# Kernel optimization log

Measured on AMD Instinct MI355X. Metric: run time of the kernel, lower is better.

Reference implementation:

```python
import jax, jax.numpy as jnp
import numpy as np

# AdEx constants (match init_kwargs)
THR = -50.4
EL = -70.6
GL = 30.0
C = 281.0
DELTAT = 2.0
V_RESET = -70.6
TAUW = 144.0
A = 4.0
B = 0.0805
DT = 1.0
N_REFRAC = 5
DAMP = 0.3
DT_GL__C = DT * GL / C
DT_A__TAUW = DT * A / TAUW

BATCH, N_IN, UNITS = 8192, 256, 1024


@jax.custom_vjp
def spike_function(v_scaled):
    return (v_scaled > 0.0).astype(jnp.float32)

def _spike_fwd(v_scaled):
    return spike_function(v_scaled), v_scaled

def _spike_bwd(v_scaled, dy):
    # pseudo-derivative: dampening * max(1 - |v_scaled|, 0)
    return (dy * DAMP * jnp.maximum(1.0 - jnp.abs(v_scaled), 0.0),)

spike_function.defvjp(_spike_fwd, _spike_bwd)


def setup_inputs() -> dict:
    key = jax.random.key(0)
    ks = jax.random.split(key, 7)
    inputs = jax.random.normal(ks[0], (BATCH, N_IN), dtype=jnp.float32)
    old_v = EL + 5.0 * jax.random.normal(ks[1], (BATCH, UNITS), dtype=jnp.float32)
    old_r = jax.random.randint(ks[2], (BATCH, UNITS), 0, N_REFRAC, dtype=jnp.int32)
    old_w = jax.random.normal(ks[3], (BATCH, UNITS), dtype=jnp.float32)
    old_z = (jax.random.uniform(ks[4], (BATCH, UNITS)) < 0.1).astype(jnp.float32)
    input_weights = jax.random.uniform(ks[5], (N_IN, UNITS), dtype=jnp.float32, minval=0.0, maxval=1.2)
    recurrent_weights = 0.7 * jax.random.normal(ks[6], (UNITS, UNITS), dtype=jnp.float32) / np.sqrt(UNITS)
    return {"inputs": inputs, "old_v": old_v, "old_r": old_r, "old_w": old_w,
            "old_z": old_z, "input_weights": input_weights,
            "recurrent_weights": recurrent_weights}


def reference(inputs, old_v, old_r, old_w, old_z, input_weights, recurrent_weights):
    units = recurrent_weights.shape[0]
    disconnect = jnp.eye(units, dtype=bool)  # no autapses on diagonal
    no_autapse_w_rec = jnp.where(disconnect, 0.0, recurrent_weights)

    i_t = inputs @ input_weights + old_z @ no_autapse_w_rec  # (B, U)

    exp_terms = jnp.clip(jnp.exp((old_v - THR) / DELTAT), -1e6, 30.0 / DT_GL__C)
    exp_terms = jax.lax.stop_gradient(exp_terms)

    new_v = (old_v - DT_GL__C * (old_v - EL)
             + DT_GL__C * DELTAT * exp_terms
             + (i_t - old_w) * DT / C)
    new_v = jnp.where(old_z > 0.5, V_RESET, new_v)

    new_w = old_w - DT / TAUW * old_w + DT_A__TAUW * (old_v - EL) + B * old_z

    is_refractory = old_r > 0
    v_scaled = -(THR - new_v) / (THR - EL)
    new_z = spike_function(v_scaled)
    new_z = jnp.where(is_refractory, 0.0, new_z)

    new_r = jnp.clip(old_r - 1 + (new_z * N_REFRAC).astype(jnp.int32), 0, N_REFRAC)

    return new_v, new_z, new_r, new_w
```

## Files before the change

kernel.cpp:

```cpp
#include <hip/hip_runtime.h>
#include <stdint.h>

#define THRC      (-50.4f)
#define ELC       (-70.6f)
#define V_RESETC  (-70.6f)
#define DT_GL_C   (0.10676156583629893f)
#define DELTATC   (2.0f)
#define DT_C      (0.0035587188612099642f)
#define DT_TAUW   (0.006944444444444444f)
#define DTA_TAUW  (0.027777777777777776f)
#define BCONST    (0.0805f)
#define EXPCLIP   (281.0f)

#define M_TOT 8192
#define UNITS 1024
#define KX    768
#define KBT   1792
#define CH    (8192*1024)
#define BM 256
#define BN 128
#define ZSLAB (M_TOT*16)

typedef __attribute__((ext_vector_type(8))) short s16x8;
typedef __attribute__((ext_vector_type(4))) float f32x4;

__device__ __forceinline__ unsigned short f2bf(float f) {
  union { float f; unsigned int u; } v; v.f = f;
  unsigned int r = v.u + 0x7fffu + ((v.u >> 16) & 1u);
  return (unsigned short)(r >> 16);
}
__device__ __forceinline__ float bf2f(unsigned short h) {
  union { unsigned int u; float f; } v; v.u = ((unsigned int)h) << 16; return v.f;
}
__device__ __forceinline__ void gload_lds16(const void* g, void* l) {
  __builtin_amdgcn_global_load_lds(
      (const __attribute__((address_space(1))) void*)g,
      (__attribute__((address_space(3))) void*)l, 16, 0, 0);
}
__device__ __forceinline__ int swz_col(int row, int k) {
  return (k & ~31) | (((((k >> 3) & 3) ^ ((row >> 1) & 3)) << 3)) | (k & 7);
}

__global__ __launch_bounds__(256) void build_ax(const float* __restrict__ X,
                                                unsigned short* __restrict__ AX) {
  int o = blockIdx.x * 256 + threadIdx.x;
  int row = o / 96;
  int c8 = (o - row * 96) * 8;
  const float* src; bool lo = false;
  if (c8 < 256)        { src = X + (size_t)row * 256 + c8; }
  else if (c8 < 512)   { src = X + (size_t)row * 256 + (c8 - 256); lo = true; }
  else                 { src = X + (size_t)row * 256 + (c8 - 512); }
  float4 f0 = *(const float4*)(src);
  float4 f1 = *(const float4*)(src + 4);
  float fv[8] = {f0.x, f0.y, f0.z, f0.w, f1.x, f1.y, f1.z, f1.w};
  unsigned short h[8];
#pragma unroll
  for (int i = 0; i < 8; ++i) {
    unsigned short hi = f2bf(fv[i]);
    h[i] = lo ? f2bf(fv[i] - bf2f(hi)) : hi;
  }
  uint4 pk;
  pk.x = (unsigned)h[0] | ((unsigned)h[1] << 16);
  pk.y = (unsigned)h[2] | ((unsigned)h[3] << 16);
  pk.z = (unsigned)h[4] | ((unsigned)h[5] << 16);
  pk.w = (unsigned)h[6] | ((unsigned)h[7] << 16);
  *(uint4*)(AX + (size_t)row * KX + swz_col(row, c8)) = pk;
}

__global__ __launch_bounds__(256) void build_b(const float* __restrict__ Wi,
                                               const float* __restrict__ Wr,
                                               unsigned short* __restrict__ BT) {
  __shared__ unsigned short tile[32][33];
  int tx = threadIdx.x & 31, ty = threadIdx.x >> 5;
  int k0 = blockIdx.x * 32, n0 = blockIdx.y * 32;
#pragma unroll
  for (int j = 0; j < 4; ++j) {
    int kk = k0 + ty + j * 8;
    int n  = n0 + tx;
    float f; bool lo = false;
    if (kk < 256)       f = Wi[(size_t)kk * 1024 + n];
    else if (kk < 512)  f = Wi[(size_t)(kk - 256) * 1024 + n];
    else if (kk < 768) { f = Wi[(size_t)(kk - 512) * 1024 + n]; lo = true; }
    else { int kr = kk - 768; f = (kr == n) ? 0.0f : Wr[(size_t)kr * 1024 + n]; }
    unsigned short h = f2bf(f);
    if (lo) h = f2bf(f - bf2f(h));
    tile[ty + j * 8][tx] = h;
  }
  __syncthreads();
#pragma unroll
  for (int j = 0; j < 4; ++j) {
    int n  = n0 + ty + j * 8;
    int kk = k0 + tx;
    BT[(size_t)n * KBT + swz_col(n, kk)] = tile[tx][ty + j * 8];
  }
}

__global__ __launch_bounds__(256) void build_zb(const float* __restrict__ Z,
                                                char* __restrict__ Zb) {
  int ge = blockIdx.x * 256 + threadIdx.x;
  float val = Z[ge];
  unsigned long long mask = __ballot(val > 0.5f);
  if ((threadIdx.x & 63) == 0) {
    int row = ge >> 10;
    int k0  = ge & 1023;
    *(unsigned long long*)(Zb + (size_t)(k0 >> 7) * ZSLAB + row * 16 + ((k0 >> 3) & 15)) = mask;
  }
}

__device__ __forceinline__ s16x8 expand_bits(unsigned zw, int l4) {
  unsigned b = zw >> (l4 * 8);
  s16x8 a;
#pragma unroll
  for (int e = 0; e < 8; ++e)
    a[e] = (short)(((b >> e) & 1u) ? 0x3F80 : 0);
  return a;
}

__global__ __launch_bounds__(512, 2) void adex_gemm(
    const unsigned short* __restrict__ AX, const unsigned short* __restrict__ BT,
    const char* __restrict__ Zb,
    const float* __restrict__ oV, const int* __restrict__ oR,
    const float* __restrict__ oW, float* __restrict__ out)
{
  __shared__ unsigned short S[2][12288];
  const int tid  = threadIdx.x;
  const int w    = tid >> 6;
  const int lane = tid & 63;
  const int l15  = lane & 15, l4 = lane >> 4;
  const int wm   = w >> 1, wn = w & 1;

  const int bid = blockIdx.x;
  const int mt = bid >> 3, nt = bid & 7;
  const int rowA0 = mt * BM;
  const int colB0 = nt * BN;

  const int srow = tid >> 2, sslot = tid & 3;
  const unsigned short* aS0 = AX + (size_t)(rowA0 + srow)       * KX  + sslot * 8;
  const unsigned short* aS1 = AX + (size_t)(rowA0 + 128 + srow) * KX  + sslot * 8;
  const unsigned short* bS  = BT + (size_t)(colB0 + srow)       * KBT + sslot * 8;

#define STAGE_A(buf)                                          \
  do { gload_lds16(aS0, &S[buf][0] + tid * 8);                \
       gload_lds16(aS1, &S[buf][0] + 4096 + tid * 8); } while (0)
#define STAGE_B(buf) gload_lds16(bS, &S[buf][0] + 8192 + tid * 8)

  const int slot = l4 ^ ((l15 >> 1) & 3);
  int offA[4], offB[4];
#pragma unroll
  for (int f = 0; f < 4; ++f) offA[f] = (wm * 64 + f * 16 + l15) * 32 + slot * 8;
#pragma unroll
  for (int f = 0; f < 4; ++f) offB[f] = 8192 + (wn * 64 + f * 16 + l15) * 32 + slot * 8;

  const char* zp0 = Zb + (size_t)(rowA0 + wm * 64 +  0 + l15) * 16;
  const char* zp1 = Zb + (size_t)(rowA0 + wm * 64 + 16 + l15) * 16;
  const char* zp2 = Zb + (size_t)(rowA0 + wm * 64 + 32 + l15) * 16;
  const char* zp3 = Zb + (size_t)(rowA0 + wm * 64 + 48 + l15) * 16;

  f32x4 acc[4][4];
#pragma unroll
  for (int i = 0; i < 4; ++i)
#pragma unroll
    for (int j = 0; j < 4; ++j) acc[i][j] = (f32x4){0.f, 0.f, 0.f, 0.f};

  STAGE_A(0); STAGE_B(0);
  uint4 zbE0 = *(const uint4*)zp0, zbE1 = *(const uint4*)zp1;
  uint4 zbE2 = *(const uint4*)zp2, zbE3 = *(const uint4*)zp3;
  asm volatile("s_waitcnt vmcnt(0)" ::: "memory");
  __syncthreads();

  int cur = 0;
#pragma unroll 2
  for (int ks = 0; ks < 24; ++ks) {
    if (ks < 23) { aS0 += 32; aS1 += 32; bS += 32; STAGE_A(cur ^ 1); STAGE_B(cur ^ 1); }
    else         { bS += 32; STAGE_B(cur ^ 1); }
    const unsigned short* base = &S[cur][0];
    s16x8 af[4], bf[4];
#pragma unroll
    for (int f = 0; f < 4; ++f) af[f] = *(const s16x8*)(base + offA[f]);
#pragma unroll
    for (int f = 0; f < 4; ++f) bf[f] = *(const s16x8*)(base + offB[f]);
#pragma unroll
    for (int i = 0; i < 4; ++i)
#pragma unroll
      for (int j = 0; j < 4; ++j)
        acc[i][j] = __builtin_amdgcn_mfma_f32_16x16x32_bf16(af[i], bf[j], acc[i][j], 0, 0, 0);
    asm volatile("s_waitcnt vmcnt(0)" ::: "memory");
    __syncthreads();
    cur ^= 1;
  }

#define ZSTEP(W0, W1, W2, W3, DOSTAGE)                                        \
  do {                                                                        \
    if (DOSTAGE) { bS += 32; STAGE_B(cur ^ 1); }                              \
    const unsigned short* base = &S[cur][0];                                  \
    s16x8 az[4];                                                              \
    az[0] = expand_bits(W0, l4); az[1] = expand_bits(W1, l4);                 \
    az[2] = expand_bits(W2, l4); az[3] = expand_bits(W3, l4);                 \
    s16x8 bf[4];                                                              \
    bf[0] = *(const s16x8*)(base + offB[0]);                                  \
    bf[1] = *(const s16x8*)(base + offB[1]);                                  \
    bf[2] = *(const s16x8*)(base + offB[2]);                                  \
    bf[3] = *(const s16x8*)(base + offB[3]);                                  \
    _Pragma("unroll")                                                         \
    for (int i = 0; i < 4; ++i)                                               \
      _Pragma("unroll")                                                       \
      for (int j = 0; j < 4; ++j)                                             \
        acc[i][j] = __builtin_amdgcn_mfma_f32_16x16x32_bf16(az[i], bf[j], acc[i][j], 0, 0, 0); \
    asm volatile("s_waitcnt vmcnt(0)" ::: "memory");                          \
    __syncthreads();                                                          \
    cur ^= 1;                                                                 \
  } while (0)

  uint4 zbO0, zbO1, zbO2, zbO3;
  for (int gp = 0; gp < 4; ++gp) {
    zp0 += ZSLAB; zp1 += ZSLAB; zp2 += ZSLAB; zp3 += ZSLAB;
    zbO0 = *(const uint4*)zp0; zbO1 = *(const uint4*)zp1;
    zbO2 = *(const uint4*)zp2; zbO3 = *(const uint4*)zp3;
    ZSTEP(zbE0.x, zbE1.x, zbE2.x, zbE3.x, true);
    ZSTEP(zbE0.y, zbE1.y, zbE2.y, zbE3.y, true);
    ZSTEP(zbE0.z, zbE1.z, zbE2.z, zbE3.z, true);
    ZSTEP(zbE0.w, zbE1.w, zbE2.w, zbE3.w, true);
    if (gp < 3) {
      zp0 += ZSLAB; zp1 += ZSLAB; zp2 += ZSLAB; zp3 += ZSLAB;
      zbE0 = *(const uint4*)zp0; zbE1 = *(const uint4*)zp1;
      zbE2 = *(const uint4*)zp2; zbE3 = *(const uint4*)zp3;
    }
    ZSTEP(zbO0.x, zbO1.x, zbO2.x, zbO3.x, true);
    ZSTEP(zbO0.y, zbO1.y, zbO2.y, zbO3.y, true);
    ZSTEP(zbO0.z, zbO1.z, zbO2.z, zbO3.z, true);
    ZSTEP(zbO0.w, zbO1.w, zbO2.w, zbO3.w, gp < 3);
  }
#undef ZSTEP
#undef STAGE_A
#undef STAGE_B

  const char* zslab = Zb + (size_t)nt * ZSLAB;
#pragma unroll
  for (int i = 0; i < 4; ++i) {
#pragma unroll
    for (int r = 0; r < 4; ++r) {
      int m = rowA0 + wm * 64 + i * 16 + l4 * 4 + r;
      unsigned zwA = *(const unsigned*)(zslab + m * 16 + (wn * 2 + 0) * 4);
      unsigned zwB = *(const unsigned*)(zslab + m * 16 + (wn * 2 + 1) * 4);
#pragma unroll
      for (int j = 0; j < 4; ++j) {
        int u = colB0 + wn * 64 + j * 16 + l15;
        size_t idx = (size_t)m * UNITS + u;
        float it = acc[i][j][r];
        unsigned zw = (j < 2) ? zwA : zwB;
        float oz = ((zw >> ((j & 1) * 16 + l15)) & 1u) ? 1.0f : 0.0f;
        float ov = oV[idx];
        float ow = oW[idx];
        int   orr = oR[idx];
        float ex = expf((ov - THRC) * 0.5f);
        ex = fminf(ex, EXPCLIP);
        float nv = ov - DT_GL_C * (ov - ELC) + (DT_GL_C * DELTATC) * ex + (it - ow) * DT_C;
        nv = (oz > 0.5f) ? V_RESETC : nv;
        float nw = ow - DT_TAUW * ow + DTA_TAUW * (ov - ELC) + BCONST * oz;
        float nz = (nv > THRC) ? 1.0f : 0.0f;
        if (orr > 0) nz = 0.0f;
        int nr = orr - 1 + (nz > 0.5f ? 5 : 0);
        nr = nr < 0 ? 0 : (nr > 5 ? 5 : nr);
        out[idx]           = nv;
        out[CH + idx]      = nz;
        out[2 * CH + idx]  = (float)nr;
        out[3 * CH + idx]  = nw;
      }
    }
  }
}

extern "C" void kernel_launch(void* const* d_in, const int* in_sizes, int n_in,
                              void* d_out, int out_size, void* d_ws, size_t ws_size,
                              hipStream_t stream) {
  const float* X  = (const float*)d_in[0];
  const float* oV = (const float*)d_in[1];
  const int*   oR = (const int*)d_in[2];
  const float* oW = (const float*)d_in[3];
  const float* oZ = (const float*)d_in[4];
  const float* Wi = (const float*)d_in[5];
  const float* Wr = (const float*)d_in[6];
  unsigned short* AX = (unsigned short*)d_ws;
  unsigned short* BT = AX + (size_t)M_TOT * KX;
  char*           Zb = (char*)(BT + (size_t)UNITS * KBT);
  float* out = (float*)d_out;

  hipLaunchKernelGGL(build_ax, dim3((M_TOT * (KX / 8)) / 256), dim3(256), 0, stream, X, AX);
  hipLaunchKernelGGL(build_b,  dim3(KBT / 32, UNITS / 32), dim3(256), 0, stream, Wi, Wr, BT);
  hipLaunchKernelGGL(build_zb, dim3((M_TOT * UNITS) / 256), dim3(256), 0, stream, oZ, Zb);
  hipLaunchKernelGGL(adex_gemm, dim3((M_TOT / BM) * (UNITS / BN)), dim3(512), 0, stream,
                     AX, BT, Zb, oV, oR, oW, out);
}
```

Before: 133.9 us.

## Load A fragments directly to registers and stage B in larger K slabs

A-operand fragments are now loaded straight from global memory into registers with inline asm instead of going through LDS, so LDS holds only B, staged four k-steps at a time from a new slab-major BT2 layout. The main loop is fully unrolled at compile time with explicit vmcnt waits and fewer barriers, one per 128-wide K slab instead of one per 32-wide step. This is meant to cut LDS traffic and barrier count and to overlap loads with MFMA more deeply. The costs are uncoalesced per-lane global loads for A, more register pressure, and hand-tuned wait counts that must match the issue order exactly.

```diff
diff --git a/kernel.cpp b/kernel.cpp
--- a/kernel.cpp
+++ b/kernel.cpp
@@ -1,5 +1,6 @@
 #include <hip/hip_runtime.h>
 #include <stdint.h>
+#include <type_traits>
 
 #define THRC      (-50.4f)
 #define ELC       (-70.6f)
@@ -15,7 +16,6 @@
 #define M_TOT 8192
 #define UNITS 1024
 #define KX    768
-#define KBT   1792
 #define CH    (8192*1024)
 #define BM 256
 #define BN 128
@@ -37,8 +37,10 @@
       (const __attribute__((address_space(1))) void*)g,
       (__attribute__((address_space(3))) void*)l, 16, 0, 0);
 }
-__device__ __forceinline__ int swz_col(int row, int k) {
-  return (k & ~31) | (((((k >> 3) & 3) ^ ((row >> 1) & 3)) << 3)) | (k & 7);
+
+template <int I, int N, typename F>
+__device__ __forceinline__ void unroll_for(F&& f) {
+  if constexpr (I < N) { f(std::integral_constant<int, I>{}); unroll_for<I + 1, N>(f); }
 }
 
 __global__ __launch_bounds__(256) void build_ax(const float* __restrict__ X,
@@ -64,12 +66,12 @@
   pk.y = (unsigned)h[2] | ((unsigned)h[3] << 16);
   pk.z = (unsigned)h[4] | ((unsigned)h[5] << 16);
   pk.w = (unsigned)h[6] | ((unsigned)h[7] << 16);
-  *(uint4*)(AX + (size_t)row * KX + swz_col(row, c8)) = pk;
+  *(uint4*)(AX + (size_t)row * KX + c8) = pk;
 }
 
 __global__ __launch_bounds__(256) void build_b(const float* __restrict__ Wi,
                                                const float* __restrict__ Wr,
-                                               unsigned short* __restrict__ BT) {
+                                               unsigned short* __restrict__ BT2) {
   __shared__ unsigned short tile[32][33];
   int tx = threadIdx.x & 31, ty = threadIdx.x >> 5;
   int k0 = blockIdx.x * 32, n0 = blockIdx.y * 32;
@@ -91,7 +93,9 @@
   for (int j = 0; j < 4; ++j) {
     int n  = n0 + ty + j * 8;
     int kk = k0 + tx;
-    BT[(size_t)n * KBT + swz_col(n, kk)] = tile[tx][ty + j * 8];
+    size_t off = (size_t)(kk >> 7) * 131072 + (size_t)((kk >> 3) & 15) * 8192
+               + (size_t)n * 8 + (kk & 7);
+    BT2[off] = tile[tx][ty + j * 8];
   }
 }
 
@@ -117,12 +121,12 @@
 }
 
 __global__ __launch_bounds__(512, 2) void adex_gemm(
-    const unsigned short* __restrict__ AX, const unsigned short* __restrict__ BT,
+    const unsigned short* __restrict__ AX, const unsigned short* __restrict__ BT2,
     const char* __restrict__ Zb,
     const float* __restrict__ oV, const int* __restrict__ oR,
     const float* __restrict__ oW, float* __restrict__ out)
 {
-  __shared__ unsigned short S[2][12288];
+  __shared__ unsigned short Bs[2][16][128][8];
   const int tid  = threadIdx.x;
   const int w    = tid >> 6;
   const int lane = tid & 63;
@@ -130,31 +134,40 @@
   const int wm   = w >> 1, wn = w & 1;
 
   const int bid = blockIdx.x;
-  const int mt = bid >> 3, nt = bid & 7;
-  const int rowA0 = mt * BM;
-  const int colB0 = nt * BN;
-
-  const int srow = tid >> 2, sslot = tid & 3;
-  const unsigned short* aS0 = AX + (size_t)(rowA0 + srow)       * KX  + sslot * 8;
-  const unsigned short* aS1 = AX + (size_t)(rowA0 + 128 + srow) * KX  + sslot * 8;
-  const unsigned short* bS  = BT + (size_t)(colB0 + srow)       * KBT + sslot * 8;
-
-#define STAGE_A(buf)                                          \
-  do { gload_lds16(aS0, &S[buf][0] + tid * 8);                \
-       gload_lds16(aS1, &S[buf][0] + 4096 + tid * 8); } while (0)
-#define STAGE_B(buf) gload_lds16(bS, &S[buf][0] + 8192 + tid * 8)
-
-  const int slot = l4 ^ ((l15 >> 1) & 3);
-  int offA[4], offB[4];
-#pragma unroll
-  for (int f = 0; f < 4; ++f) offA[f] = (wm * 64 + f * 16 + l15) * 32 + slot * 8;
-#pragma unroll
-  for (int f = 0; f < 4; ++f) offB[f] = 8192 + (wn * 64 + f * 16 + l15) * 32 + slot * 8;
+  const int nt = bid & 7, mt = bid >> 3;
+  const int rowA0 = mt * BM, colB0 = nt * BN;
+
+  const unsigned short* bSrc = BT2 + (size_t)(tid >> 7) * 8192
+                             + ((size_t)colB0 + (tid & 127)) * 8;
+  char* bDst = (char*)&Bs[0][0][0][0] + tid * 16;
+
+#define STAGE_B(buf, ss)                                                     \
+  do {                                                                       \
+    const unsigned short* s_ = bSrc + (size_t)(ss) * 131072;                 \
+    char* d_ = bDst + (buf) * 32768;                                         \
+    gload_lds16(s_,         d_);                                             \
+    gload_lds16(s_ + 32768, d_ + 8192);                                      \
+    gload_lds16(s_ + 65536, d_ + 16384);                                     \
+    gload_lds16(s_ + 98304, d_ + 24576);                                     \
+  } while (0)
+
+  const unsigned short* pA0 = AX + (size_t)(rowA0 + wm * 64 +  0 + l15) * KX + l4 * 8;
+  const unsigned short* pA1 = AX + (size_t)(rowA0 + wm * 64 + 16 + l15) * KX + l4 * 8;
+  const unsigned short* pA2 = AX + (size_t)(rowA0 + wm * 64 + 32 + l15) * KX + l4 * 8;
+  const unsigned short* pA3 = AX + (size_t)(rowA0 + wm * 64 + 48 + l15) * KX + l4 * 8;
+
+#define LD(dst, ptr, off)                                        \
+  asm volatile("global_load_dwordx4 %0, %1, off offset:%2"       \
+               : "=v"(dst) : "v"(ptr), "n"(off) : "memory")
+#define LDZ(dst, ptr)                                            \
+  asm volatile("global_load_dwordx4 %0, %1, off"                 \
+               : "=v"(dst) : "v"(ptr) : "memory")
 
   const char* zp0 = Zb + (size_t)(rowA0 + wm * 64 +  0 + l15) * 16;
   const char* zp1 = Zb + (size_t)(rowA0 + wm * 64 + 16 + l15) * 16;
   const char* zp2 = Zb + (size_t)(rowA0 + wm * 64 + 32 + l15) * 16;
   const char* zp3 = Zb + (size_t)(rowA0 + wm * 64 + 48 + l15) * 16;
+  uint4 zr0, zr1, zr2, zr3;
 
   f32x4 acc[4][4];
 #pragma unroll
@@ -162,77 +175,99 @@
 #pragma unroll
     for (int j = 0; j < 4; ++j) acc[i][j] = (f32x4){0.f, 0.f, 0.f, 0.f};
 
-  STAGE_A(0); STAGE_B(0);
-  uint4 zbE0 = *(const uint4*)zp0, zbE1 = *(const uint4*)zp1;
-  uint4 zbE2 = *(const uint4*)zp2, zbE3 = *(const uint4*)zp3;
-  asm volatile("s_waitcnt vmcnt(0)" ::: "memory");
-  __syncthreads();
-
-  int cur = 0;
-#pragma unroll 2
-  for (int ks = 0; ks < 24; ++ks) {
-    if (ks < 23) { aS0 += 32; aS1 += 32; bS += 32; STAGE_A(cur ^ 1); STAGE_B(cur ^ 1); }
-    else         { bS += 32; STAGE_B(cur ^ 1); }
-    const unsigned short* base = &S[cur][0];
-    s16x8 af[4], bf[4];
-#pragma unroll
-    for (int f = 0; f < 4; ++f) af[f] = *(const s16x8*)(base + offA[f]);
-#pragma unroll
-    for (int f = 0; f < 4; ++f) bf[f] = *(const s16x8*)(base + offB[f]);
-#pragma unroll
-    for (int i = 0; i < 4; ++i)
-#pragma unroll
-      for (int j = 0; j < 4; ++j)
-        acc[i][j] = __builtin_amdgcn_mfma_f32_16x16x32_bf16(af[i], bf[j], acc[i][j], 0, 0, 0);
-    asm volatile("s_waitcnt vmcnt(0)" ::: "memory");
-    __syncthreads();
-    cur ^= 1;
-  }
-
-#define ZSTEP(W0, W1, W2, W3, DOSTAGE)                                        \
-  do {                                                                        \
-    if (DOSTAGE) { bS += 32; STAGE_B(cur ^ 1); }                              \
-    const unsigned short* base = &S[cur][0];                                  \
-    s16x8 az[4];                                                              \
-    az[0] = expand_bits(W0, l4); az[1] = expand_bits(W1, l4);                 \
-    az[2] = expand_bits(W2, l4); az[3] = expand_bits(W3, l4);                 \
-    s16x8 bf[4];                                                              \
-    bf[0] = *(const s16x8*)(base + offB[0]);                                  \
-    bf[1] = *(const s16x8*)(base + offB[1]);                                  \
-    bf[2] = *(const s16x8*)(base + offB[2]);                                  \
-    bf[3] = *(const s16x8*)(base + offB[3]);                                  \
-    _Pragma("unroll")                                                         \
-    for (int i = 0; i < 4; ++i)                                               \
-      _Pragma("unroll")                                                       \
-      for (int j = 0; j < 4; ++j)                                             \
-        acc[i][j] = __builtin_amdgcn_mfma_f32_16x16x32_bf16(az[i], bf[j], acc[i][j], 0, 0, 0); \
-    asm volatile("s_waitcnt vmcnt(0)" ::: "memory");                          \
-    __syncthreads();                                                          \
-    cur ^= 1;                                                                 \
+#define MFMA16(a0,a1,a2,a3, b0,b1,b2,b3)                                        \
+  do {                                                                          \
+    acc[0][0]=__builtin_amdgcn_mfma_f32_16x16x32_bf16(a0,b0,acc[0][0],0,0,0);   \
+    acc[0][1]=__builtin_amdgcn_mfma_f32_16x16x32_bf16(a0,b1,acc[0][1],0,0,0);   \
+    acc[0][2]=__builtin_amdgcn_mfma_f32_16x16x32_bf16(a0,b2,acc[0][2],0,0,0);   \
+    acc[0][3]=__builtin_amdgcn_mfma_f32_16x16x32_bf16(a0,b3,acc[0][3],0,0,0);   \
+    acc[1][0]=__builtin_amdgcn_mfma_f32_16x16x32_bf16(a1,b0,acc[1][0],0,0,0);   \
+    acc[1][1]=__builtin_amdgcn_mfma_f32_16x16x32_bf16(a1,b1,acc[1][1],0,0,0);   \
+    acc[1][2]=__builtin_amdgcn_mfma_f32_16x16x32_bf16(a1,b2,acc[1][2],0,0,0);   \
+    acc[1][3]=__builtin_amdgcn_mfma_f32_16x16x32_bf16(a1,b3,acc[1][3],0,0,0);   \
+    acc[2][0]=__builtin_amdgcn_mfma_f32_16x16x32_bf16(a2,b0,acc[2][0],0,0,0);   \
+    acc[2][1]=__builtin_amdgcn_mfma_f32_16x16x32_bf16(a2,b1,acc[2][1],0,0,0);   \
+    acc[2][2]=__builtin_amdgcn_mfma_f32_16x16x32_bf16(a2,b2,acc[2][2],0,0,0);   \
+    acc[2][3]=__builtin_amdgcn_mfma_f32_16x16x32_bf16(a2,b3,acc[2][3],0,0,0);   \
+    acc[3][0]=__builtin_amdgcn_mfma_f32_16x16x32_bf16(a3,b0,acc[3][0],0,0,0);   \
+    acc[3][1]=__builtin_amdgcn_mfma_f32_16x16x32_bf16(a3,b1,acc[3][1],0,0,0);   \
+    acc[3][2]=__builtin_amdgcn_mfma_f32_16x16x32_bf16(a3,b2,acc[3][2],0,0,0);   \
+    acc[3][3]=__builtin_amdgcn_mfma_f32_16x16x32_bf16(a3,b3,acc[3][3],0,0,0);   \
   } while (0)
 
-  uint4 zbO0, zbO1, zbO2, zbO3;
-  for (int gp = 0; gp < 4; ++gp) {
-    zp0 += ZSLAB; zp1 += ZSLAB; zp2 += ZSLAB; zp3 += ZSLAB;
-    zbO0 = *(const uint4*)zp0; zbO1 = *(const uint4*)zp1;
-    zbO2 = *(const uint4*)zp2; zbO3 = *(const uint4*)zp3;
-    ZSTEP(zbE0.x, zbE1.x, zbE2.x, zbE3.x, true);
-    ZSTEP(zbE0.y, zbE1.y, zbE2.y, zbE3.y, true);
-    ZSTEP(zbE0.z, zbE1.z, zbE2.z, zbE3.z, true);
-    ZSTEP(zbE0.w, zbE1.w, zbE2.w, zbE3.w, true);
-    if (gp < 3) {
+#define BREAD(bf, buf, ksc)                                                     \
+  do {                                                                          \
+    const unsigned short* bb_ = &Bs[buf][0][0][0] + ((ksc) * 4 + l4) * 1024     \
+                              + (wn * 64 + l15) * 8;                            \
+    bf[0] = *(const s16x8*)(bb_);                                               \
+    bf[1] = *(const s16x8*)(bb_ + 128);                                         \
+    bf[2] = *(const s16x8*)(bb_ + 256);                                         \
+    bf[3] = *(const s16x8*)(bb_ + 384);                                         \
+  } while (0)
+
+  s16x8 fa[2][4];
+
+  STAGE_B(0, 0);
+  LD(fa[0][0], pA0, 0); LD(fa[0][1], pA1, 0);
+  LD(fa[0][2], pA2, 0); LD(fa[0][3], pA3, 0);
+  asm volatile("s_waitcnt vmcnt(4)" ::: "memory");
+  __builtin_amdgcn_sched_barrier(0);
+  __builtin_amdgcn_s_barrier();
+
+  unroll_for<0, 24>([&](auto G) {
+    constexpr int g = decltype(G)::value;
+    constexpr int ks = g & 3, ss = g >> 2, buf = ss & 1, cur = g & 1;
+    if constexpr (g + 1 < 24) {
+      constexpr int imm = (g + 1) * 64;
+      LD(fa[cur ^ 1][0], pA0, imm); LD(fa[cur ^ 1][1], pA1, imm);
+      LD(fa[cur ^ 1][2], pA2, imm); LD(fa[cur ^ 1][3], pA3, imm);
+    } else {
+      LDZ(zr0, zp0); LDZ(zr1, zp1); LDZ(zr2, zp2); LDZ(zr3, zp3);
       zp0 += ZSLAB; zp1 += ZSLAB; zp2 += ZSLAB; zp3 += ZSLAB;
-      zbE0 = *(const uint4*)zp0; zbE1 = *(const uint4*)zp1;
-      zbE2 = *(const uint4*)zp2; zbE3 = *(const uint4*)zp3;
     }
-    ZSTEP(zbO0.x, zbO1.x, zbO2.x, zbO3.x, true);
-    ZSTEP(zbO0.y, zbO1.y, zbO2.y, zbO3.y, true);
-    ZSTEP(zbO0.z, zbO1.z, zbO2.z, zbO3.z, true);
-    ZSTEP(zbO0.w, zbO1.w, zbO2.w, zbO3.w, gp < 3);
-  }
-#undef ZSTEP
-#undef STAGE_A
+    if constexpr (ks == 1) STAGE_B(buf ^ 1, ss + 1);
+    asm volatile("s_waitcnt vmcnt(%0)" :: "n"((ks == 0 || ks == 3) ? 4 : 8) : "memory");
+    __builtin_amdgcn_sched_barrier(0);
+    s16x8 bf[4];
+    BREAD(bf, buf, ks);
+    MFMA16(fa[cur][0], fa[cur][1], fa[cur][2], fa[cur][3], bf[0], bf[1], bf[2], bf[3]);
+    if constexpr (ks == 3) __builtin_amdgcn_s_barrier();
+  });
+
+  unroll_for<0, 8>([&](auto ZG) {
+    constexpr int zg = decltype(ZG)::value;
+    constexpr int ss = 6 + zg, buf = ss & 1;
+    if constexpr (zg < 7) STAGE_B(buf ^ 1, ss + 1);
+    asm volatile("s_waitcnt vmcnt(%0)" :: "n"(zg < 7 ? 4 : 0) : "memory");
+    __builtin_amdgcn_sched_barrier(0);
+    {
+      s16x8 az0, az1, az2, az3, bf[4];
+      az0 = expand_bits(zr0.x, l4); az1 = expand_bits(zr1.x, l4);
+      az2 = expand_bits(zr2.x, l4); az3 = expand_bits(zr3.x, l4);
+      BREAD(bf, buf, 0); MFMA16(az0, az1, az2, az3, bf[0], bf[1], bf[2], bf[3]);
+      az0 = expand_bits(zr0.y, l4); az1 = expand_bits(zr1.y, l4);
+      az2 = expand_bits(zr2.y, l4); az3 = expand_bits(zr3.y, l4);
+      BREAD(bf, buf, 1); MFMA16(az0, az1, az2, az3, bf[0], bf[1], bf[2], bf[3]);
+      az0 = expand_bits(zr0.z, l4); az1 = expand_bits(zr1.z, l4);
+      az2 = expand_bits(zr2.z, l4); az3 = expand_bits(zr3.z, l4);
+      BREAD(bf, buf, 2); MFMA16(az0, az1, az2, az3, bf[0], bf[1], bf[2], bf[3]);
+      az0 = expand_bits(zr0.w, l4); az1 = expand_bits(zr1.w, l4);
+      az2 = expand_bits(zr2.w, l4); az3 = expand_bits(zr3.w, l4);
+      BREAD(bf, buf, 3); MFMA16(az0, az1, az2, az3, bf[0], bf[1], bf[2], bf[3]);
+    }
+    if constexpr (zg < 7) {
+      LDZ(zr0, zp0); LDZ(zr1, zp1); LDZ(zr2, zp2); LDZ(zr3, zp3);
+      zp0 += ZSLAB; zp1 += ZSLAB; zp2 += ZSLAB; zp3 += ZSLAB;
+      asm volatile("s_waitcnt vmcnt(4)" ::: "memory");
+      __builtin_amdgcn_sched_barrier(0);
+      __builtin_amdgcn_s_barrier();
+    }
+  });
 #undef STAGE_B
+#undef LD
+#undef LDZ
+#undef MFMA16
+#undef BREAD
 
   const char* zslab = Zb + (size_t)nt * ZSLAB;
 #pragma unroll
@@ -280,14 +315,14 @@
   const float* oZ = (const float*)d_in[4];
   const float* Wi = (const float*)d_in[5];
   const float* Wr = (const float*)d_in[6];
-  unsigned short* AX = (unsigned short*)d_ws;
-  unsigned short* BT = AX + (size_t)M_TOT * KX;
-  char*           Zb = (char*)(BT + (size_t)UNITS * KBT);
+  unsigned short* AX  = (unsigned short*)d_ws;
+  unsigned short* BT2 = AX + (size_t)M_TOT * KX;
+  char*           Zb  = (char*)(BT2 + (size_t)UNITS * 1792);
   float* out = (float*)d_out;
 
   hipLaunchKernelGGL(build_ax, dim3((M_TOT * (KX / 8)) / 256), dim3(256), 0, stream, X, AX);
-  hipLaunchKernelGGL(build_b,  dim3(KBT / 32, UNITS / 32), dim3(256), 0, stream, Wi, Wr, BT);
+  hipLaunchKernelGGL(build_b,  dim3(1792 / 32, UNITS / 32), dim3(256), 0, stream, Wi, Wr, BT2);
   hipLaunchKernelGGL(build_zb, dim3((M_TOT * UNITS) / 256), dim3(256), 0, stream, oZ, Zb);
   hipLaunchKernelGGL(adex_gemm, dim3((M_TOT / BM) * (UNITS / BN)), dim3(512), 0, stream,
-                     AX, BT, Zb, oV, oR, oW, out);
-}
+                     AX, BT2, Zb, oV, oR, oW, out);
+}
```

Result: no change. 132.2 us (-1.3%).
